# Kernel optimization log

Measured on AMD Instinct MI355X. Metric: run time of the kernel, lower is better.

Reference implementation:

```python
import jax, jax.numpy as jnp
import numpy as np

N_NODES = 20000
N_EDGES = 160000
N_GRAPHS = 64
X_DIM = 9
E_DIM = 1
U_RAW = 4096
U_DIM = 256
E_HID = 1024
E_OUT = 512
N_HID = 512
N_OUT = 1


def _lin_params(k, fan_in, fan_out):
    kw, kb = jax.random.split(k)
    bound = 1.0 / np.sqrt(fan_in)
    W = jax.random.uniform(kw, (fan_in, fan_out), jnp.float32, -bound, bound)
    b = jax.random.uniform(kb, (fan_out,), jnp.float32, -bound, bound)
    return W, b


def setup_inputs() -> dict:
    key = jax.random.key(0)
    ks = jax.random.split(key, 16)
    x = jax.random.normal(ks[0], (N_NODES, X_DIM), jnp.float32)
    edge_attr = jax.random.normal(ks[1], (N_EDGES, E_DIM), jnp.float32)
    u = jax.random.normal(ks[2], (N_GRAPHS, U_RAW), jnp.float32)
    edge_index = jax.random.randint(ks[3], (2, N_EDGES), 0, N_NODES, jnp.int64)
    batch = jax.random.randint(ks[4], (N_NODES,), 0, N_GRAPHS, jnp.int64)

    Wsel, bsel = _lin_params(ks[5], U_RAW, U_DIM)
    e_in = E_DIM + 2 * X_DIM + U_DIM  # 275
    eW1, eb1 = _lin_params(ks[6], e_in, E_HID)
    eW2, eb2 = _lin_params(ks[7], E_HID, E_HID)
    eW3, eb3 = _lin_params(ks[8], E_HID, E_HID)
    eW4, eb4 = _lin_params(ks[9], E_HID, E_HID)
    eW5, eb5 = _lin_params(ks[10], E_HID, E_OUT)
    n1W1, n1b1 = _lin_params(ks[11], E_OUT + X_DIM, N_HID)  # 521
    n1W2, n1b2 = _lin_params(ks[12], N_HID, N_HID)
    n2W1, n2b1 = _lin_params(ks[13], X_DIM + N_HID + U_DIM, N_HID)  # 777
    n2W2, n2b2 = _lin_params(ks[14], N_HID, N_OUT)

    return dict(x=x, edge_attr=edge_attr, u=u, edge_index=edge_index, batch=batch,
                Wsel=Wsel, bsel=bsel,
                eW1=eW1, eb1=eb1, eW2=eW2, eb2=eb2, eW3=eW3, eb3=eb3,
                eW4=eW4, eb4=eb4, eW5=eW5, eb5=eb5,
                n1W1=n1W1, n1b1=n1b1, n1W2=n1W2, n1b2=n1b2,
                n2W1=n2W1, n2b1=n2b1, n2W2=n2W2, n2b2=n2b2)


def _forward(x, edge_attr, u, edge_index, batch,
             Wsel, bsel, eW1, eb1, eW2, eb2, eW3, eb3, eW4, eb4, eW5, eb5,
             n1W1, n1b1, n1W2, n1b2, n2W1, n2b1, n2W2, n2b2):
    relu = jax.nn.relu
    u2 = u @ Wsel + bsel  # [B, 256]
    row, col = edge_index[0], edge_index[1]

    # EdgeModel: cat([src, dest, edge_attr, u[batch[row]]]) -> 5-layer MLP
    e = jnp.concatenate([x[row], x[col], edge_attr, u2[batch[row]]], axis=1)
    e = relu(e @ eW1 + eb1)
    e = relu(e @ eW2 + eb2)
    e = relu(e @ eW3 + eb3)
    e = relu(e @ eW4 + eb4)
    e = e @ eW5 + eb5  # [E, 512]

    # NodeModel: gather x[col], MLP1, scatter_mean over row, MLP2
    h = jnp.concatenate([x[col], e], axis=1)
    h = relu(h @ n1W1 + n1b1)
    h = relu(h @ n1W2 + n1b2)  # [E, 512]
    ssum = jax.ops.segment_sum(h, row, num_segments=x.shape[0])
    cnt = jax.ops.segment_sum(jnp.ones((h.shape[0],), h.dtype), row, num_segments=x.shape[0])
    agg = ssum / jnp.maximum(cnt, 1.0)[:, None]  # scatter_mean

    z = jnp.concatenate([x, agg, u2[batch]], axis=1)
    z = relu(z @ n2W1 + n2b1)
    z = z @ n2W2 + n2b2  # [N, 1]
    return jnp.squeeze(z)


def reference(x, edge_attr, u, edge_index, batch,
              Wsel, bsel, eW1, eb1, eW2, eb2, eW3, eb3, eW4, eb4, eW5, eb5,
              n1W1, n1b1, n1W2, n1b2, n2W1, n2b1, n2W2, n2b2):
    return _forward(x, edge_attr, u, edge_index, batch,
                    Wsel, bsel, eW1, eb1, eW2, eb2, eW3, eb3, eW4, eb4, eW5, eb5,
                    n1W1, n1b1, n1W2, n1b2, n2W1, n2b1, n2W2, n2b2)
```

## Files before the change

kernel.cpp:

```cpp
#include <hip/hip_runtime.h>

typedef _Float16 f16;
typedef __attribute__((ext_vector_type(8))) _Float16 f16x8;
typedef __attribute__((ext_vector_type(4))) float f32x4;

#define E_TOTAL 160000
#define NN 20000
#define NGRAPH 64

__device__ __forceinline__ void gl_lds16(const void* g, void* l) {
    __builtin_amdgcn_global_load_lds((const __attribute__((address_space(1))) void*)g,
                                     (__attribute__((address_space(3))) void*)l, 16, 0, 0);
}

#define MFMA16(a, b, c) __builtin_amdgcn_mfma_f32_16x16x32_f16((a), (b), (c), 0, 0, 0)
#define LGKM0 do { asm volatile("s_waitcnt lgkmcnt(0)" ::: "memory"); \
                   __builtin_amdgcn_sched_barrier(0); } while (0)
#define VMW4  asm volatile("s_waitcnt vmcnt(4)" ::: "memory")
#define VMW0  asm volatile("s_waitcnt vmcnt(0)" ::: "memory")
#define SBAR  __builtin_amdgcn_s_barrier()

template <int RELU, int AUXU, int AUXX, int SCAT>
__global__ __launch_bounds__(512, 2) void hgemm8(
    int M, int N, int K,
    const f16* __restrict__ A, int lda,
    const f16* __restrict__ Bt,
    f16* __restrict__ C, int ldc,
    const float* __restrict__ bias,
    const f16* __restrict__ utab, const int* __restrict__ uidx,
    const float* __restrict__ x9, const int* __restrict__ xidx, const float* __restrict__ W9,
    float* __restrict__ sout, const int* __restrict__ sidx)
{
    __shared__ __align__(16) char Ash[2][2][16384];
    __shared__ __align__(16) char Bsh[2][2][16384];
    __shared__ float Ws9[AUXX ? 2304 : 1];

    const int tid  = threadIdx.x;
    const int lane = tid & 63;
    const int w    = tid >> 6;

    const int nbn = gridDim.x;
    const int nwg = nbn * gridDim.y;
    {
    }
    int d  = blockIdx.y * nbn + blockIdx.x;
    int q8 = nwg >> 3, r8 = nwg & 7;
    int xk = d & 7, j8 = d >> 3;
    int wl = (xk < r8 ? xk * (q8 + 1) : r8 * (q8 + 1) + (xk - r8) * q8) + j8;
    const int bm = (wl / nbn) * 256;
    const int bn = (wl % nbn) * 256;

    const int wm = (w >> 2) * 128;
    const int wn = (w & 3) * 64;
    const int fr = lane & 15;
    const int kq = lane >> 4;

    const char* Ab = (const char*)A;
    const char* Bb = (const char*)Bt;
    const size_t lda2 = (size_t)lda * 2;
    const size_t ldb2 = (size_t)K * 2;

    f32x4 acc[8][4] = {};

    int aoff[8], boff[4];
#pragma unroll
    for (int mi = 0; mi < 8; ++mi) {
        int r = wm + mi * 16 + fr;
        aoff[mi] = r * 64 + ((kq ^ ((r >> 1) & 3)) << 4);
    }
#pragma unroll
    for (int ni = 0; ni < 4; ++ni) {
        int r = wn + ni * 16 + fr;
        boff[ni] = r * 64 + ((kq ^ ((r >> 1) & 3)) << 4);
    }

    int sdest[2];
    size_t gsrcA[2], gsrcB[2];
#pragma unroll
    for (int i = 0; i < 2; ++i) {
        int L = i * 8192 + tid * 16;
        int row = L >> 6;
        int s = (L >> 4) & 3;
        int sw = (s ^ ((row >> 1) & 3)) << 4;
        sdest[i] = L;
        gsrcA[i] = (size_t)(bm + row) * lda2 + sw;
        gsrcB[i] = (size_t)(bn + row) * ldb2 + sw;
    }

    const int NT = K >> 6;

    auto stageA = [&](int t, int h, int buf) {
        size_t kb = (size_t)t * 128 + h * 64;
#pragma unroll
        for (int i = 0; i < 2; ++i)
            gl_lds16(Ab + gsrcA[i] + kb, &Ash[buf][h][0] + sdest[i]);
    };
    auto stageB = [&](int t, int h, int buf) {
        size_t kb = (size_t)t * 128 + h * 64;
#pragma unroll
        for (int i = 0; i < 2; ++i)
            gl_lds16(Bb + gsrcB[i] + kb, &Bsh[buf][h][0] + sdest[i]);
    };

    stageA(0, 0, 0); stageB(0, 0, 0); stageA(0, 1, 0); stageB(0, 1, 0);
    VMW4;
    SBAR;

    for (int t = 0; t < NT; ++t) {
        const int cur = t & 1, nxt = cur ^ 1;
        const bool pre = (t + 1 < NT);
        const char* A0 = &Ash[cur][0][0];
        const char* A1 = &Ash[cur][1][0];
        const char* B0 = &Bsh[cur][0][0];
        const char* B1 = &Bsh[cur][1][0];

        f16x8 a0[4], b0[4];
#pragma unroll
        for (int i = 0; i < 4; ++i) a0[i] = *(const f16x8*)(A0 + aoff[i]);
#pragma unroll
        for (int i = 0; i < 4; ++i) b0[i] = *(const f16x8*)(B0 + boff[i]);
        if (pre) stageA(t + 1, 0, nxt);
        SBAR;
        LGKM0;
        __builtin_amdgcn_s_setprio(1);
#pragma unroll
        for (int mi = 0; mi < 4; ++mi)
#pragma unroll
            for (int ni = 0; ni < 4; ++ni)
                acc[mi][ni] = MFMA16(a0[mi], b0[ni], acc[mi][ni]);
        __builtin_amdgcn_s_setprio(0);
        SBAR;

        f16x8 a1[4];
#pragma unroll
        for (int i = 0; i < 4; ++i) a1[i] = *(const f16x8*)(A0 + aoff[4 + i]);
        if (pre) stageB(t + 1, 0, nxt);
        SBAR;
        LGKM0;
        __builtin_amdgcn_s_setprio(1);
#pragma unroll
        for (int mi = 0; mi < 4; ++mi)
#pragma unroll
            for (int ni = 0; ni < 4; ++ni)
                acc[4 + mi][ni] = MFMA16(a1[mi], b0[ni], acc[4 + mi][ni]);
        __builtin_amdgcn_s_setprio(0);
        if (pre) { VMW4; } else { VMW0; }
        SBAR;

        f16x8 a2[4], b2[4];
#pragma unroll
        for (int i = 0; i < 4; ++i) a2[i] = *(const f16x8*)(A1 + aoff[i]);
#pragma unroll
        for (int i = 0; i < 4; ++i) b2[i] = *(const f16x8*)(B1 + boff[i]);
        if (pre) stageA(t + 1, 1, nxt);
        SBAR;
        LGKM0;
        __builtin_amdgcn_s_setprio(1);
#pragma unroll
        for (int mi = 0; mi < 4; ++mi)
#pragma unroll
            for (int ni = 0; ni < 4; ++ni)
                acc[mi][ni] = MFMA16(a2[mi], b2[ni], acc[mi][ni]);
        __builtin_amdgcn_s_setprio(0);
        SBAR;

        f16x8 a3[4];
#pragma unroll
        for (int i = 0; i < 4; ++i) a3[i] = *(const f16x8*)(A1 + aoff[4 + i]);
        if (pre) stageB(t + 1, 1, nxt);
        SBAR;
        LGKM0;
        __builtin_amdgcn_s_setprio(1);
#pragma unroll
        for (int mi = 0; mi < 4; ++mi)
#pragma unroll
            for (int ni = 0; ni < 4; ++ni)
                acc[4 + mi][ni] = MFMA16(a3[mi], b2[ni], acc[4 + mi][ni]);
        __builtin_amdgcn_s_setprio(0);
        if (pre) { VMW4; }
        SBAR;
    }

    if (AUXX) {
        for (int i = tid; i < 9 * 256; i += 512)
            Ws9[i] = W9[(size_t)(i >> 8) * N + bn + (i & 255)];
        __syncthreads();
    }

#pragma unroll
    for (int mi = 0; mi < 8; ++mi) {
        int r0 = bm + wm + mi * 16 + kq * 4;
#pragma unroll
        for (int r = 0; r < 4; ++r) {
            int grow = r0 + r;
            if (grow >= M) continue;
            int ub = 0;
            if (AUXU) ub = uidx[grow];
            int sb = 0;
            if (SCAT) sb = sidx[grow];
            float xv[9];
            if (AUXX) {
                int xi = xidx ? xidx[grow] : grow;
#pragma unroll
                for (int q = 0; q < 9; ++q) xv[q] = x9[(size_t)xi * 9 + q];
            }
#pragma unroll
            for (int ni = 0; ni < 4; ++ni) {
                int lcol = wn + ni * 16 + fr;
                int col = bn + lcol;
                float v = acc[mi][ni][r] + bias[col];
                if (AUXU) v += (float)utab[(size_t)ub * N + col];
                if (AUXX) {
                    float s = 0.f;
#pragma unroll
                    for (int q = 0; q < 9; ++q) s = fmaf(xv[q], Ws9[q * 256 + lcol], s);
                    v += s;
                }
                if (RELU) v = fmaxf(v, 0.f);
                if (SCAT) {
                    atomicAdd(sout + (size_t)sb * N + col, v);
                } else {
                    C[(size_t)grow * ldc + col] = (f16)v;
                }
            }
        }
    }
}

__global__ void k_wt(const float* __restrict__ W, f16* __restrict__ Wt,
                     int r0, int Ksub, int N, int Kp)
{
    size_t t = (size_t)blockIdx.x * 256 + threadIdx.x;
    if (t >= (size_t)N * Kp) return;
    int n = (int)(t / Kp), k = (int)(t % Kp);
    Wt[t] = (k < Ksub) ? (f16)W[(size_t)(r0 + k) * N + n] : (f16)0.f;
}

__global__ void k_cvt(const float* __restrict__ W, f16* __restrict__ Wt, int n)
{
    int t = blockIdx.x * 256 + threadIdx.x;
    if (t < n) Wt[t] = (f16)W[t];
}

__global__ void k_cbias(const float* __restrict__ n1W1, const float* __restrict__ eb5,
                        const float* __restrict__ n1b1, float* __restrict__ cb)
{
    int b = blockIdx.x * 256 + threadIdx.x;
    if (b >= 512) return;
    float s = n1b1[b];
    for (int c = 0; c < 512; ++c) s = fmaf(eb5[c], n1W1[(size_t)(9 + c) * 512 + b], s);
    cb[b] = s;
}

__global__ __launch_bounds__(256) void k_u2(const float* __restrict__ u,
                                            const float* __restrict__ Wsel,
                                            const float* __restrict__ bsel,
                                            f16* __restrict__ u2h)
{
    __shared__ float us[4096];
    __shared__ float red[4][64];
    const int g = blockIdx.y;
    const int c0 = blockIdx.x * 64;
    const int col = threadIdx.x & 63;
    const int kp = threadIdx.x >> 6;
    for (int i = threadIdx.x; i < 4096; i += 256) us[i] = u[(size_t)g * 4096 + i];
    __syncthreads();
    float acc = 0.f;
    for (int k = kp * 1024; k < kp * 1024 + 1024; ++k)
        acc = fmaf(us[k], Wsel[(size_t)k * 256 + c0 + col], acc);
    red[kp][col] = acc;
    __syncthreads();
    if (kp == 0) {
        float v = red[0][col] + red[1][col] + red[2][col] + red[3][col] + bsel[c0 + col];
        u2h[(size_t)g * 256 + c0 + col] = (f16)v;
    }
}

__global__ void k_gather19(int e0, int Ce,
                           const float* __restrict__ x, const float* __restrict__ eattr,
                           const int* __restrict__ ei, const int* __restrict__ batch,
                           f16* __restrict__ feat, int* __restrict__ ebat)
{
    size_t t = (size_t)blockIdx.x * 256 + threadIdx.x;
    if (t >= (size_t)Ce * 64) return;
    int i = (int)(t >> 6), j = (int)(t & 63);
    int e = e0 + i;
    float v = 0.f;
    if (j < 9)        v = x[ei[e] * 9 + j];
    else if (j < 18)  v = x[ei[E_TOTAL + e] * 9 + (j - 9)];
    else if (j == 18) v = eattr[e];
    else if (j == 19) ebat[i] = batch[ei[e]];
    feat[t] = (f16)v;
}

__global__ void k_cnt(const int* __restrict__ ei, float* __restrict__ cnt)
{
    int t = blockIdx.x * 256 + threadIdx.x;
    if (t < E_TOTAL) atomicAdd(cnt + ei[t], 1.0f);
}

__global__ void k_agg(const float* __restrict__ ssum, const float* __restrict__ cnt,
                      f16* __restrict__ agg)
{
    size_t t = (size_t)blockIdx.x * 256 + threadIdx.x;
    if (t >= (size_t)NN * 512) return;
    int n = (int)(t >> 9);
    agg[t] = (f16)(ssum[t] / fmaxf(cnt[n], 1.f));
}

__global__ void k_final(const f16* __restrict__ z1, const float* __restrict__ W,
                        const float* __restrict__ b, float* __restrict__ out)
{
    int gt = blockIdx.x * 256 + threadIdx.x;
    int row = gt >> 6;
    int lane = threadIdx.x & 63;
    if (row >= NN) return;
    float s = 0.f;
#pragma unroll
    for (int c = lane; c < 512; c += 64) s += (float)z1[(size_t)row * 512 + c] * W[c];
#pragma unroll
    for (int off = 32; off; off >>= 1) s += __shfl_down(s, off);
    if (lane == 0) out[row] = s + b[0];
}


extern "C" void kernel_launch(void* const* d_in, const int* in_sizes, int n_in,
                              void* d_out, int out_size, void* d_ws, size_t ws_size,
                              hipStream_t stream)
{
    const float* x     = (const float*)d_in[0];
    const float* eattr = (const float*)d_in[1];
    const float* u     = (const float*)d_in[2];
    const int*   ei    = (const int*)d_in[3];
    const int*   batch = (const int*)d_in[4];
    const float* Wsel  = (const float*)d_in[5];
    const float* bsel  = (const float*)d_in[6];
    const float* eW1 = (const float*)d_in[7],  * eb1 = (const float*)d_in[8];
    const float* eW2 = (const float*)d_in[9],  * eb2 = (const float*)d_in[10];
    const float* eW3 = (const float*)d_in[11], * eb3 = (const float*)d_in[12];
    const float* eW4 = (const float*)d_in[13], * eb4 = (const float*)d_in[14];
    const float* eW5 = (const float*)d_in[15], * eb5 = (const float*)d_in[16];
    const float* n1W1 = (const float*)d_in[17], * n1b1 = (const float*)d_in[18];
    const float* n1W2 = (const float*)d_in[19], * n1b2 = (const float*)d_in[20];
    const float* n2W1 = (const float*)d_in[21], * n2b1 = (const float*)d_in[22];
    const float* n2W2 = (const float*)d_in[23], * n2b2 = (const float*)d_in[24];
    float* out = (float*)d_out;

    char* ws = (char*)d_ws;
    size_t off = 0;
    auto alc = [&](size_t bytes) { char* p = ws + off; off += (bytes + 255) & ~(size_t)255; return p; };

    float* ssum  = (float*)alc((size_t)NN * 512 * 4);
    float* cnt   = (float*)alc((size_t)NN * 4);
    float* zbias = (float*)alc(1024 * 4);
    float* cbias = (float*)alc(512 * 4);
    f16* u2h     = (f16*)alc((size_t)256 * 256 * 2);
    f16* ubias_e = (f16*)alc((size_t)64 * 1024 * 2);
    f16* ubias_n = (f16*)alc((size_t)64 * 512 * 2);
    f16* eW1t19  = (f16*)alc((size_t)1024 * 64 * 2);
    f16* eW1ut   = (f16*)alc((size_t)1024 * 256 * 2);
    f16* eW2t    = (f16*)alc((size_t)1024 * 1024 * 2);
    f16* eW3t    = (f16*)alc((size_t)1024 * 1024 * 2);
    f16* eW4t    = (f16*)alc((size_t)1024 * 1024 * 2);
    f16* eW5h    = (f16*)alc((size_t)1024 * 512 * 2);
    f16* combo_t = (f16*)alc((size_t)512 * 1024 * 2);
    f16* n1W1et  = (f16*)alc((size_t)512 * 512 * 2);
    f16* n1W2t   = (f16*)alc((size_t)512 * 512 * 2);
    f16* n2W1et  = (f16*)alc((size_t)512 * 512 * 2);
    f16* n2W1ut  = (f16*)alc((size_t)512 * 256 * 2);
    f16* agg     = (f16*)alc((size_t)20224 * 512 * 2);
    f16* z1      = (f16*)alc((size_t)20224 * 512 * 2);
    size_t fixed = off;

    size_t per_edge = 64 * 2 + 1024 * 2 + 1024 * 2 + 4;
    size_t avail = ws_size > fixed ? ws_size - fixed : 0;
    long long Cmax = (long long)(avail / per_edge);
    int C;
    if (Cmax >= E_TOTAL)      C = E_TOTAL;
    else if (Cmax >= 16384)   C = (int)((Cmax / 16384) * 16384);
    else                      C = (int)((Cmax / 256) * 256);
    if (C < 256) C = 256;

    f16* featc = (f16*)(ws + fixed);
    f16* buf1  = featc + (size_t)C * 64;
    f16* buf2  = buf1 + (size_t)C * 1024;
    int* ebat  = (int*)(buf2 + (size_t)C * 1024);

    size_t zlen = (size_t)((char*)zbias - (char*)ssum) + 1024 * 4;
    hipMemsetAsync(ssum, 0, zlen, stream);

    auto wt = [&](const float* W, f16* Wt, int r0, int Ksub, int N, int Kp) {
        size_t tot = (size_t)N * Kp;
        k_wt<<<(unsigned)((tot + 255) / 256), 256, 0, stream>>>(W, Wt, r0, Ksub, N, Kp);
    };
    wt(eW1, eW1t19, 0, 19, 1024, 64);
    wt(eW1, eW1ut, 19, 256, 1024, 256);
    wt(eW2, eW2t, 0, 1024, 1024, 1024);
    wt(eW3, eW3t, 0, 1024, 1024, 1024);
    wt(eW4, eW4t, 0, 1024, 1024, 1024);
    wt(n1W1, n1W1et, 9, 512, 512, 512);
    wt(n1W2, n1W2t, 0, 512, 512, 512);
    wt(n2W1, n2W1et, 9, 512, 512, 512);
    wt(n2W1, n2W1ut, 521, 256, 512, 256);
    k_cvt<<<(1024 * 512 + 255) / 256, 256, 0, stream>>>(eW5, eW5h, 1024 * 512);

    k_u2<<<dim3(4, NGRAPH), 256, 0, stream>>>(u, Wsel, bsel, u2h);
    k_cnt<<<(E_TOTAL + 255) / 256, 256, 0, stream>>>(ei, cnt);
    k_cbias<<<2, 256, 0, stream>>>(n1W1, eb5, n1b1, cbias);

    hgemm8<0,0,0,0><<<dim3(4, 1), 512, 0, stream>>>(64, 1024, 256, u2h, 256, eW1ut,
        ubias_e, 1024, eb1, nullptr, nullptr, nullptr, nullptr, nullptr, nullptr, nullptr);
    hgemm8<0,0,0,0><<<dim3(2, 1), 512, 0, stream>>>(64, 512, 256, u2h, 256, n2W1ut,
        ubias_n, 512, n2b1, nullptr, nullptr, nullptr, nullptr, nullptr, nullptr, nullptr);

    hgemm8<0,0,0,0><<<dim3(4, 2), 512, 0, stream>>>(512, 1024, 512, n1W1et, 512, eW5h,
        combo_t, 1024, zbias, nullptr, nullptr, nullptr, nullptr, nullptr, nullptr, nullptr);

    for (int e0 = 0; e0 < E_TOTAL; e0 += C) {
        int Ce = E_TOTAL - e0 < C ? E_TOTAL - e0 : C;
        int gy = (Ce + 255) / 256;

        k_gather19<<<(unsigned)(((size_t)Ce * 64 + 255) / 256), 256, 0, stream>>>(
            e0, Ce, x, eattr, ei, batch, featc, ebat);

        hgemm8<1,1,0,0><<<dim3(4, gy), 512, 0, stream>>>(Ce, 1024, 64, featc, 64, eW1t19,
            buf1, 1024, zbias, ubias_e, ebat, nullptr, nullptr, nullptr, nullptr, nullptr);
        hgemm8<1,0,0,0><<<dim3(4, gy), 512, 0, stream>>>(Ce, 1024, 1024, buf1, 1024, eW2t,
            buf2, 1024, eb2, nullptr, nullptr, nullptr, nullptr, nullptr, nullptr, nullptr);
        hgemm8<1,0,0,0><<<dim3(4, gy), 512, 0, stream>>>(Ce, 1024, 1024, buf2, 1024, eW3t,
            buf1, 1024, eb3, nullptr, nullptr, nullptr, nullptr, nullptr, nullptr, nullptr);
        hgemm8<1,0,0,0><<<dim3(4, gy), 512, 0, stream>>>(Ce, 1024, 1024, buf1, 1024, eW4t,
            buf2, 1024, eb4, nullptr, nullptr, nullptr, nullptr, nullptr, nullptr, nullptr);

        hgemm8<1,0,1,0><<<dim3(2, gy), 512, 0, stream>>>(Ce, 512, 1024, buf2, 1024, combo_t,
            buf1, 512, cbias, nullptr, nullptr, x, ei + E_TOTAL + e0, n1W1, nullptr, nullptr);

        hgemm8<1,0,0,1><<<dim3(2, gy), 512, 0, stream>>>(Ce, 512, 512, buf1, 512, n1W2t,
            nullptr, 512, n1b2, nullptr, nullptr, nullptr, nullptr, nullptr, ssum, ei + e0);
    }

    k_agg<<<(unsigned)(((size_t)NN * 512 + 255) / 256), 256, 0, stream>>>(ssum, cnt, agg);
    hgemm8<1,1,1,0><<<dim3(2, 79), 512, 0, stream>>>(NN, 512, 512, agg, 512, n2W1et,
        z1, 512, zbias, ubias_n, batch, x, nullptr, n2W1, nullptr, nullptr);
    k_final<<<(NN * 64 + 255) / 256, 256, 0, stream>>>(z1, n2W2, n2b2, out);
}
```

Measured before the change: 2.279 ms.

## Software-pipeline LDS fragment loads, batch weight conversion, hoist edge gather

The GEMM main loop now loads the next LDS fragments (a1, a2/b2, and next-tile a0/b0) before the MFMA block that precedes them, using partial lgkmcnt waits so LDS reads overlap with matrix math. Separately, the ten weight-conversion launches are merged into one multi-job kernel, the u2 projection kernel is re-split into more blocks with a tree reduction, and the edge feature gather is done once for all edges outside the chunk loop. The agg/z1 buffers are aliased onto the edge workspace to save memory. The trade-off is more live fragment registers and more barriers per iteration, and the partial-wait ordering has to stay correct.

```diff
diff --git a/kernel.cpp b/kernel.cpp
--- a/kernel.cpp
+++ b/kernel.cpp
@@ -14,11 +14,12 @@
 }
 
 #define MFMA16(a, b, c) __builtin_amdgcn_mfma_f32_16x16x32_f16((a), (b), (c), 0, 0, 0)
-#define LGKM0 do { asm volatile("s_waitcnt lgkmcnt(0)" ::: "memory"); \
-                   __builtin_amdgcn_sched_barrier(0); } while (0)
+#define LGKM(n) do { asm volatile("s_waitcnt lgkmcnt(" #n ")" ::: "memory"); \
+                     __builtin_amdgcn_sched_barrier(0); } while (0)
 #define VMW4  asm volatile("s_waitcnt vmcnt(4)" ::: "memory")
 #define VMW0  asm volatile("s_waitcnt vmcnt(0)" ::: "memory")
 #define SBAR  __builtin_amdgcn_s_barrier()
+#define SCHED0 __builtin_amdgcn_sched_barrier(0)
 
 template <int RELU, int AUXU, int AUXX, int SCAT>
 __global__ __launch_bounds__(512, 2) void hgemm8(
@@ -41,8 +42,6 @@
 
     const int nbn = gridDim.x;
     const int nwg = nbn * gridDim.y;
-    {
-    }
     int d  = blockIdx.y * nbn + blockIdx.x;
     int q8 = nwg >> 3, r8 = nwg & 7;
     int xk = d & 7, j8 = d >> 3;
@@ -102,26 +101,28 @@
             gl_lds16(Bb + gsrcB[i] + kb, &Bsh[buf][h][0] + sdest[i]);
     };
 
+    f16x8 a0[4], b0[4], a1[4], a2[4], b2[4], a3[4];
+
     stageA(0, 0, 0); stageB(0, 0, 0); stageA(0, 1, 0); stageB(0, 1, 0);
     VMW4;
     SBAR;
+#pragma unroll
+    for (int i = 0; i < 4; ++i) a0[i] = *(const f16x8*)(&Ash[0][0][0] + aoff[i]);
+#pragma unroll
+    for (int i = 0; i < 4; ++i) b0[i] = *(const f16x8*)(&Bsh[0][0][0] + boff[i]);
 
     for (int t = 0; t < NT; ++t) {
         const int cur = t & 1, nxt = cur ^ 1;
         const bool pre = (t + 1 < NT);
         const char* A0 = &Ash[cur][0][0];
         const char* A1 = &Ash[cur][1][0];
-        const char* B0 = &Bsh[cur][0][0];
         const char* B1 = &Bsh[cur][1][0];
 
-        f16x8 a0[4], b0[4];
-#pragma unroll
-        for (int i = 0; i < 4; ++i) a0[i] = *(const f16x8*)(A0 + aoff[i]);
-#pragma unroll
-        for (int i = 0; i < 4; ++i) b0[i] = *(const f16x8*)(B0 + boff[i]);
+#pragma unroll
+        for (int i = 0; i < 4; ++i) a1[i] = *(const f16x8*)(A0 + aoff[4 + i]);
         if (pre) stageA(t + 1, 0, nxt);
         SBAR;
-        LGKM0;
+        LGKM(4);
         __builtin_amdgcn_s_setprio(1);
 #pragma unroll
         for (int mi = 0; mi < 4; ++mi)
@@ -131,12 +132,16 @@
         __builtin_amdgcn_s_setprio(0);
         SBAR;
 
-        f16x8 a1[4];
-#pragma unroll
-        for (int i = 0; i < 4; ++i) a1[i] = *(const f16x8*)(A0 + aoff[4 + i]);
         if (pre) stageB(t + 1, 0, nxt);
         SBAR;
-        LGKM0;
+        LGKM(0);
+        if (pre) { VMW4; } else { VMW0; }
+        SBAR;
+#pragma unroll
+        for (int i = 0; i < 4; ++i) a2[i] = *(const f16x8*)(A1 + aoff[i]);
+#pragma unroll
+        for (int i = 0; i < 4; ++i) b2[i] = *(const f16x8*)(B1 + boff[i]);
+        SCHED0;
         __builtin_amdgcn_s_setprio(1);
 #pragma unroll
         for (int mi = 0; mi < 4; ++mi)
@@ -144,17 +149,13 @@
             for (int ni = 0; ni < 4; ++ni)
                 acc[4 + mi][ni] = MFMA16(a1[mi], b0[ni], acc[4 + mi][ni]);
         __builtin_amdgcn_s_setprio(0);
-        if (pre) { VMW4; } else { VMW0; }
-        SBAR;
-
-        f16x8 a2[4], b2[4];
-#pragma unroll
-        for (int i = 0; i < 4; ++i) a2[i] = *(const f16x8*)(A1 + aoff[i]);
-#pragma unroll
-        for (int i = 0; i < 4; ++i) b2[i] = *(const f16x8*)(B1 + boff[i]);
+        SBAR;
+
+#pragma unroll
+        for (int i = 0; i < 4; ++i) a3[i] = *(const f16x8*)(A1 + aoff[4 + i]);
         if (pre) stageA(t + 1, 1, nxt);
         SBAR;
-        LGKM0;
+        LGKM(4);
         __builtin_amdgcn_s_setprio(1);
 #pragma unroll
         for (int mi = 0; mi < 4; ++mi)
@@ -164,12 +165,20 @@
         __builtin_amdgcn_s_setprio(0);
         SBAR;
 
-        f16x8 a3[4];
-#pragma unroll
-        for (int i = 0; i < 4; ++i) a3[i] = *(const f16x8*)(A1 + aoff[4 + i]);
         if (pre) stageB(t + 1, 1, nxt);
         SBAR;
-        LGKM0;
+        LGKM(0);
+        if (pre) {
+            VMW4;
+            SBAR;
+            const char* An = &Ash[nxt][0][0];
+            const char* Bn = &Bsh[nxt][0][0];
+#pragma unroll
+            for (int i = 0; i < 4; ++i) a0[i] = *(const f16x8*)(An + aoff[i]);
+#pragma unroll
+            for (int i = 0; i < 4; ++i) b0[i] = *(const f16x8*)(Bn + boff[i]);
+            SCHED0;
+        }
         __builtin_amdgcn_s_setprio(1);
 #pragma unroll
         for (int mi = 0; mi < 4; ++mi)
@@ -177,7 +186,6 @@
             for (int ni = 0; ni < 4; ++ni)
                 acc[4 + mi][ni] = MFMA16(a3[mi], b2[ni], acc[4 + mi][ni]);
         __builtin_amdgcn_s_setprio(0);
-        if (pre) { VMW4; }
         SBAR;
     }
 
@@ -227,19 +235,21 @@
     }
 }
 
-__global__ void k_wt(const float* __restrict__ W, f16* __restrict__ Wt,
-                     int r0, int Ksub, int N, int Kp)
-{
+struct WtJob { const float* src; f16* dst; int r0, ks, n, kp, tr; };
+struct WtJobs { WtJob j[10]; };
+
+__global__ void k_wtall(WtJobs js)
+{
+    WtJob jb = js.j[blockIdx.y];
+    size_t tot = (size_t)jb.n * jb.kp;
     size_t t = (size_t)blockIdx.x * 256 + threadIdx.x;
-    if (t >= (size_t)N * Kp) return;
-    int n = (int)(t / Kp), k = (int)(t % Kp);
-    Wt[t] = (k < Ksub) ? (f16)W[(size_t)(r0 + k) * N + n] : (f16)0.f;
-}
-
-__global__ void k_cvt(const float* __restrict__ W, f16* __restrict__ Wt, int n)
-{
-    int t = blockIdx.x * 256 + threadIdx.x;
-    if (t < n) Wt[t] = (f16)W[t];
+    if (t >= tot) return;
+    if (jb.tr) {
+        int n = (int)(t / jb.kp), k = (int)(t % jb.kp);
+        jb.dst[t] = (k < jb.ks) ? (f16)jb.src[(size_t)(jb.r0 + k) * jb.n + n] : (f16)0.f;
+    } else {
+        jb.dst[t] = (f16)jb.src[t];
+    }
 }
 
 __global__ void k_cbias(const float* __restrict__ n1W1, const float* __restrict__ eb5,
@@ -252,44 +262,47 @@
     cb[b] = s;
 }
 
-__global__ __launch_bounds__(256) void k_u2(const float* __restrict__ u,
-                                            const float* __restrict__ Wsel,
-                                            const float* __restrict__ bsel,
-                                            f16* __restrict__ u2h)
+__global__ __launch_bounds__(256) void k_u2b(const float* __restrict__ u,
+                                             const float* __restrict__ Wsel,
+                                             const float* __restrict__ bsel,
+                                             f16* __restrict__ u2h)
 {
     __shared__ float us[4096];
-    __shared__ float red[4][64];
+    __shared__ float red[256];
     const int g = blockIdx.y;
-    const int c0 = blockIdx.x * 64;
-    const int col = threadIdx.x & 63;
-    const int kp = threadIdx.x >> 6;
+    const int c0 = blockIdx.x * 16;
+    const int col = threadIdx.x & 15;
+    const int kp = threadIdx.x >> 4;
     for (int i = threadIdx.x; i < 4096; i += 256) us[i] = u[(size_t)g * 4096 + i];
     __syncthreads();
     float acc = 0.f;
-    for (int k = kp * 1024; k < kp * 1024 + 1024; ++k)
-        acc = fmaf(us[k], Wsel[(size_t)k * 256 + c0 + col], acc);
-    red[kp][col] = acc;
+    const float* wp = Wsel + (size_t)(kp * 256) * 256 + c0 + col;
+#pragma unroll 8
+    for (int i = 0; i < 256; ++i) acc = fmaf(us[kp * 256 + i], wp[(size_t)i * 256], acc);
+    red[threadIdx.x] = acc;
     __syncthreads();
-    if (kp == 0) {
-        float v = red[0][col] + red[1][col] + red[2][col] + red[3][col] + bsel[c0 + col];
-        u2h[(size_t)g * 256 + c0 + col] = (f16)v;
-    }
-}
-
-__global__ void k_gather19(int e0, int Ce,
-                           const float* __restrict__ x, const float* __restrict__ eattr,
+    if (kp < 8) red[threadIdx.x] += red[threadIdx.x + 128];
+    __syncthreads();
+    if (kp < 4) red[threadIdx.x] += red[threadIdx.x + 64];
+    __syncthreads();
+    if (kp < 2) red[threadIdx.x] += red[threadIdx.x + 32];
+    __syncthreads();
+    if (kp == 0)
+        u2h[(size_t)g * 256 + c0 + col] = (f16)(red[threadIdx.x] + red[threadIdx.x + 16] + bsel[c0 + col]);
+}
+
+__global__ void k_gather19(const float* __restrict__ x, const float* __restrict__ eattr,
                            const int* __restrict__ ei, const int* __restrict__ batch,
                            f16* __restrict__ feat, int* __restrict__ ebat)
 {
     size_t t = (size_t)blockIdx.x * 256 + threadIdx.x;
-    if (t >= (size_t)Ce * 64) return;
+    if (t >= (size_t)E_TOTAL * 64) return;
     int i = (int)(t >> 6), j = (int)(t & 63);
-    int e = e0 + i;
     float v = 0.f;
-    if (j < 9)        v = x[ei[e] * 9 + j];
-    else if (j < 18)  v = x[ei[E_TOTAL + e] * 9 + (j - 9)];
-    else if (j == 18) v = eattr[e];
-    else if (j == 19) ebat[i] = batch[ei[e]];
+    if (j < 9)        v = x[ei[i] * 9 + j];
+    else if (j < 18)  v = x[ei[E_TOTAL + i] * 9 + (j - 9)];
+    else if (j == 18) v = eattr[i];
+    else if (j == 19) ebat[i] = batch[ei[i]];
     feat[t] = (f16)v;
 }
 
@@ -368,45 +381,47 @@
     f16* n1W2t   = (f16*)alc((size_t)512 * 512 * 2);
     f16* n2W1et  = (f16*)alc((size_t)512 * 512 * 2);
     f16* n2W1ut  = (f16*)alc((size_t)512 * 256 * 2);
-    f16* agg     = (f16*)alc((size_t)20224 * 512 * 2);
-    f16* z1      = (f16*)alc((size_t)20224 * 512 * 2);
+    f16* featAll = (f16*)alc((size_t)E_TOTAL * 64 * 2);
+    int* ebatAll = (int*)alc((size_t)E_TOTAL * 4);
     size_t fixed = off;
 
-    size_t per_edge = 64 * 2 + 1024 * 2 + 1024 * 2 + 4;
+    size_t per_edge = 4096;
+    size_t need_ro = (size_t)20224 * 512 * 2 * 2;
     size_t avail = ws_size > fixed ? ws_size - fixed : 0;
     long long Cmax = (long long)(avail / per_edge);
     int C;
     if (Cmax >= E_TOTAL)      C = E_TOTAL;
     else if (Cmax >= 16384)   C = (int)((Cmax / 16384) * 16384);
     else                      C = (int)((Cmax / 256) * 256);
-    if (C < 256) C = 256;
-
-    f16* featc = (f16*)(ws + fixed);
-    f16* buf1  = featc + (size_t)C * 64;
-    f16* buf2  = buf1 + (size_t)C * 1024;
-    int* ebat  = (int*)(buf2 + (size_t)C * 1024);
-
-    size_t zlen = (size_t)((char*)zbias - (char*)ssum) + 1024 * 4;
+    if ((size_t)C * per_edge < need_ro)
+        C = (int)(((need_ro + per_edge - 1) / per_edge + 255) / 256 * 256);
+
+    f16* buf1 = (f16*)(ws + fixed);
+    f16* buf2 = buf1 + (size_t)C * 1024;
+    f16* agg  = (f16*)(ws + fixed);
+    f16* z1   = agg + (size_t)20224 * 512;
+
+    size_t zlen = (size_t)((char*)cbias - (char*)ssum) + 512 * 4;
     hipMemsetAsync(ssum, 0, zlen, stream);
 
-    auto wt = [&](const float* W, f16* Wt, int r0, int Ksub, int N, int Kp) {
-        size_t tot = (size_t)N * Kp;
-        k_wt<<<(unsigned)((tot + 255) / 256), 256, 0, stream>>>(W, Wt, r0, Ksub, N, Kp);
-    };
-    wt(eW1, eW1t19, 0, 19, 1024, 64);
-    wt(eW1, eW1ut, 19, 256, 1024, 256);
-    wt(eW2, eW2t, 0, 1024, 1024, 1024);
-    wt(eW3, eW3t, 0, 1024, 1024, 1024);
-    wt(eW4, eW4t, 0, 1024, 1024, 1024);
-    wt(n1W1, n1W1et, 9, 512, 512, 512);
-    wt(n1W2, n1W2t, 0, 512, 512, 512);
-    wt(n2W1, n2W1et, 9, 512, 512, 512);
-    wt(n2W1, n2W1ut, 521, 256, 512, 256);
-    k_cvt<<<(1024 * 512 + 255) / 256, 256, 0, stream>>>(eW5, eW5h, 1024 * 512);
-
-    k_u2<<<dim3(4, NGRAPH), 256, 0, stream>>>(u, Wsel, bsel, u2h);
+    WtJobs js;
+    js.j[0] = {eW1,  eW1t19, 0,   19,   1024, 64,   1};
+    js.j[1] = {eW1,  eW1ut,  19,  256,  1024, 256,  1};
+    js.j[2] = {eW2,  eW2t,   0,   1024, 1024, 1024, 1};
+    js.j[3] = {eW3,  eW3t,   0,   1024, 1024, 1024, 1};
+    js.j[4] = {eW4,  eW4t,   0,   1024, 1024, 1024, 1};
+    js.j[5] = {n1W1, n1W1et, 9,   512,  512,  512,  1};
+    js.j[6] = {n1W2, n1W2t,  0,   512,  512,  512,  1};
+    js.j[7] = {n2W1, n2W1et, 9,   512,  512,  512,  1};
+    js.j[8] = {n2W1, n2W1ut, 521, 256,  512,  256,  1};
+    js.j[9] = {eW5,  eW5h,   0,   0,    1024, 512,  0};
+    k_wtall<<<dim3(4096, 10), 256, 0, stream>>>(js);
+
+    k_u2b<<<dim3(16, NGRAPH), 256, 0, stream>>>(u, Wsel, bsel, u2h);
     k_cnt<<<(E_TOTAL + 255) / 256, 256, 0, stream>>>(ei, cnt);
     k_cbias<<<2, 256, 0, stream>>>(n1W1, eb5, n1b1, cbias);
+    k_gather19<<<(unsigned)(((size_t)E_TOTAL * 64 + 255) / 256), 256, 0, stream>>>(
+        x, eattr, ei, batch, featAll, ebatAll);
 
     hgemm8<0,0,0,0><<<dim3(4, 1), 512, 0, stream>>>(64, 1024, 256, u2h, 256, eW1ut,
         ubias_e, 1024, eb1, nullptr, nullptr, nullptr, nullptr, nullptr, nullptr, nullptr);
@@ -420,11 +435,9 @@
         int Ce = E_TOTAL - e0 < C ? E_TOTAL - e0 : C;
         int gy = (Ce + 255) / 256;
 
-        k_gather19<<<(unsigned)(((size_t)Ce * 64 + 255) / 256), 256, 0, stream>>>(
-            e0, Ce, x, eattr, ei, batch, featc, ebat);
-
-        hgemm8<1,1,0,0><<<dim3(4, gy), 512, 0, stream>>>(Ce, 1024, 64, featc, 64, eW1t19,
-            buf1, 1024, zbias, ubias_e, ebat, nullptr, nullptr, nullptr, nullptr, nullptr);
+        hgemm8<1,1,0,0><<<dim3(4, gy), 512, 0, stream>>>(Ce, 1024, 64,
+            featAll + (size_t)e0 * 64, 64, eW1t19,
+            buf1, 1024, zbias, ubias_e, ebatAll + e0, nullptr, nullptr, nullptr, nullptr, nullptr);
         hgemm8<1,0,0,0><<<dim3(4, gy), 512, 0, stream>>>(Ce, 1024, 1024, buf1, 1024, eW2t,
             buf2, 1024, eb2, nullptr, nullptr, nullptr, nullptr, nullptr, nullptr, nullptr);
         hgemm8<1,0,0,0><<<dim3(4, gy), 512, 0, stream>>>(Ce, 1024, 1024, buf2, 1024, eW3t,
```

Result: faster. 2.213 ms (-2.9%).
